# Optimization experiments

Hardware: AMD Instinct MI355X
Metric: run time of the kernel (lower is better)

## Reference

```python
import jax, jax.numpy as jnp
import numpy as np

B, N, IN, OUT, H = 8, 256, 256, 256, 4
HD = OUT // H  # 64
ALPHA = 0.2    # LeakyReLU negative slope
EPS = 1e-5


def layernorm(x, g, b):
    m = x.mean(-1, keepdims=True)
    v = jnp.mean(jnp.square(x - m), axis=-1, keepdims=True)
    return (x - m) / jnp.sqrt(v + EPS) * g + b


def setup_inputs() -> dict:
    key = jax.random.key(0)
    ks = jax.random.split(key, 16)
    s = 0.05
    return {
        'h':    jax.random.normal(ks[0], (B, N, IN), jnp.float32),
        'adj':  jax.random.randint(ks[1], (B, N, N), 0, 2, jnp.int32),
        # per-head params (leading dim H)
        'W':    jax.random.normal(ks[2], (H, IN, HD), jnp.float32) * s,      # node proj (no bias)
        'We1':  jax.random.normal(ks[3], (H, 2 * IN, HD), jnp.float32) * s,  # edge_encoder lin
        'be1':  jnp.zeros((H, HD), jnp.float32),
        'Wa1':  jax.random.normal(ks[4], (H, 3 * HD, HD), jnp.float32) * s,  # attn mlp lin1
        'ba1':  jnp.zeros((H, HD), jnp.float32),
        'wa2':  jax.random.normal(ks[5], (H, HD), jnp.float32) * s,          # attn mlp lin2 -> scalar
        'ba2':  jnp.zeros((H,), jnp.float32),
        'ln_g': jnp.ones((H, HD), jnp.float32),   # per-head LayerNorm
        'ln_b': jnp.zeros((H, HD), jnp.float32),
        'Wo':   jax.random.normal(ks[6], (OUT, OUT), jnp.float32) * s,       # output projection
        'bo':   jnp.zeros((OUT,), jnp.float32),
        'ln2_g': jnp.ones((OUT,), jnp.float32),   # final LayerNorm
        'ln2_b': jnp.zeros((OUT,), jnp.float32),
    }


def _head(h, adj_mask, W, We1, be1, Wa1, ba1, wa2, ba2, g, b):
    # h: [B,N,IN]; adj_mask: [B,N,N] bool (True where adj==0)
    Wh = jnp.einsum('bnf,fd->bnd', h, W)                      # [B,N,HD]
    # attention MLP lin1 applied to concat([Wh_i, Wh_j, edge]):
    # split weight so the per-node parts are computed once, broadcast over pairs
    Wa, Wb, We = Wa1[:HD], Wa1[HD:2 * HD], Wa1[2 * HD:]
    si = jnp.einsum('bnd,de->bne', Wh, Wa) + ba1              # [B,N,HD]
    sj = jnp.einsum('bnd,de->bne', Wh, Wb)                    # [B,N,HD]
    # edge encoder: Linear(cat[h_i,h_j]) -> leaky_relu, split likewise
    ei = jnp.einsum('bnf,fd->bnd', h, We1[:IN]) + be1         # [B,N,HD]
    ej = jnp.einsum('bnf,fd->bnd', h, We1[IN:])               # [B,N,HD]
    edge = jax.nn.leaky_relu(ei[:, :, None, :] + ej[:, None, :, :], ALPHA)  # [B,N,N,HD]
    hidden = jax.nn.leaky_relu(
        si[:, :, None, :] + sj[:, None, :, :] + jnp.einsum('bijd,de->bije', edge, We),
        ALPHA)                                                # [B,N,N,HD]
    e = jnp.einsum('bijd,d->bij', hidden, wa2) + ba2          # [B,N,N]
    e = jnp.where(adj_mask, -1e9, e)
    attn = jax.nn.softmax(e, axis=-1)                         # [B,N,N]
    hp = jnp.einsum('bij,bjd->bid', attn, Wh)                 # [B,N,HD]
    return layernorm(hp, g, b)


def reference(h, adj, W, We1, be1, Wa1, ba1, wa2, ba2, ln_g, ln_b, Wo, bo, ln2_g, ln2_b):
    adj_mask = (adj == 0)
    heads = [
        _head(h, adj_mask, W[i], We1[i], be1[i], Wa1[i], ba1[i],
              wa2[i], ba2[i], ln_g[i], ln_b[i])
        for i in range(H)
    ]
    concat = jnp.concatenate(heads, axis=-1)                  # [B,N,OUT]
    out = jnp.einsum('bnf,fo->bno', concat, Wo) + bo
    out = out + h                                             # residual (IN == OUT)
    return layernorm(out, ln2_g, ln2_b)
```

## Files before the change

### kernel.cpp

```cpp
#include <hip/hip_runtime.h>
#include <hip/hip_bf16.h>

#define B_ 8
#define N_ 256
#define IN_ 256
#define OUT_ 256
#define H_ 4
#define HD_ 64
#define ALPHA_ 0.2f
#define EPS_ 1e-5f

#define S_ (B_*H_*N_*HD_)


typedef unsigned short ushort_t;
typedef __attribute__((ext_vector_type(8))) short short8;
typedef __attribute__((ext_vector_type(4))) float floatx4;

__device__ __forceinline__ float lrelu(float x) { return fmaxf(x, ALPHA_ * x); }
__device__ __forceinline__ ushort_t f2b(float x) {
    unsigned u = __float_as_uint(x);
    unsigned r = ((u >> 16) & 1u) + 0x7fffu;
    return (ushort_t)((u + r) >> 16);
}
__device__ __forceinline__ unsigned pk2(float x0, float x1) {
    __hip_bfloat162 p = __float22bfloat162_rn(make_float2(x0, x1));
    return *(unsigned*)&p;
}

__global__ __launch_bounds__(256) void build_kernel(
    const float* __restrict__ W, const float* __restrict__ We1,
    const float* __restrict__ Wa1, const float* __restrict__ Wo,
    ushort_t* __restrict__ wfull, ushort_t* __restrict__ wo_t,
    ushort_t* __restrict__ bw_b)
{
    const int blk = blockIdx.x;
    const int tid = threadIdx.x;
    const int r4 = tid >> 6, cl = tid & 63;

    if (blk < 48) {
        const int hh = blk / 12, rem = blk % 12;
        const int cq = rem >> 2, ft = rem & 3;
        const int f0 = ft * 64;
        __shared__ float tl[64][65];
        for (int r = r4; r < 64; r += 4) {
            float v;
            if (cq == 0)      v = W  [((size_t)hh * 256 + f0 + r) * 64 + cl];
            else if (cq == 1) v = We1[((size_t)hh * 512 + f0 + r) * 64 + cl];
            else              v = We1[((size_t)hh * 512 + 256 + f0 + r) * 64 + cl];
            tl[r][cl] = v;
        }
        __syncthreads();
        for (int cr = r4; cr < 64; cr += 4)
            wfull[((size_t)hh * 256 + cq * 64 + cr) * 256 + f0 + cl] = f2b(tl[cl][cr]);
    } else if (blk < 64) {
        const int mm = blk - 48;
        const int hh = mm >> 2, ft = mm & 3;
        const int f0 = ft * 64;
        __shared__ float wlds[64][65];
        __shared__ float wa_l[64][65];
        __shared__ float tl[64][65];
        for (int r = r4; r < 64; r += 4) {
            wlds[r][cl] = W[((size_t)hh * 256 + f0 + r) * 64 + cl];
            wa_l[r][cl] = Wa1[((size_t)hh * 192 + r) * 64 + cl];
        }
        __syncthreads();
        for (int f = r4; f < 64; f += 4) {
            float acc = 0.f;
            #pragma unroll 8
            for (int g = 0; g < 64; ++g) acc += wlds[f][g] * wa_l[g][cl];
            tl[f][cl] = acc;
        }
        __syncthreads();
        for (int cr = r4; cr < 64; cr += 4)
            wfull[((size_t)hh * 256 + 192 + cr) * 256 + f0 + cl] = f2b(tl[cl][cr]);
    } else if (blk < 80) {
        const int bb = blk - 64;
        const int to = bb & 3, tf = bb >> 2;
        __shared__ float t[64][65];
        for (int rr = r4; rr < 64; rr += 4)
            t[rr][cl] = Wo[(size_t)(tf * 64 + rr) * 256 + to * 64 + cl];
        __syncthreads();
        for (int rr = r4; rr < 64; rr += 4)
            wo_t[(size_t)(to * 64 + rr) * 256 + tf * 64 + cl] = f2b(t[cl][rr]);
    } else {
        const int hh = blk - 80;
        for (int idx = tid; idx < 64 * 128; idx += 256) {
            const int e = idx >> 7, k = idx & 127;
            const int row = (k < 64) ? (128 + k) : k;
            bw_b[hh * 8192 + idx] = f2b(Wa1[(size_t)hh * 192 * 64 + row * 64 + e]);
        }
    }
}

__global__ __launch_bounds__(256) void prep2_kernel(
    const float* __restrict__ h, const ushort_t* __restrict__ wfull,
    const float* __restrict__ be1, const float* __restrict__ ba1,
    float* __restrict__ ws)
{
    const int gm = blockIdx.x & 127, gn = blockIdx.x >> 7;
    const int tid = threadIdx.x, lane = tid & 63, wid = tid >> 6;
    const int quad = lane >> 4, l15 = lane & 15;

    float*    ei_f = ws;
    float*    si_f = ws + S_;
    ushort_t* ej_b = (ushort_t*)(ws + 2 * (size_t)S_);
    ushort_t* Wh_b = ej_b + S_;

    floatx4 acc[2];
    #pragma unroll
    for (int nt = 0; nt < 2; ++nt) acc[nt] = (floatx4){0.f,0.f,0.f,0.f};

    #pragma unroll 2
    for (int ks = 0; ks < 8; ++ks) {
        const float* hp0 = &h[(size_t)(gm * 16 + l15) * 256 + ks * 32 + quad * 8];
        float4 a0 = *(const float4*)hp0;
        float4 a1 = *(const float4*)(hp0 + 4);
        union { unsigned u[4]; short8 s; } aw;
        aw.u[0] = pk2(a0.x, a0.y); aw.u[1] = pk2(a0.z, a0.w);
        aw.u[2] = pk2(a1.x, a1.y); aw.u[3] = pk2(a1.z, a1.w);
        #pragma unroll
        for (int nt = 0; nt < 2; ++nt) {
            short8 bfr = *(const short8*)&wfull[(size_t)(gn * 128 + wid * 32 + nt * 16 + l15) * 256 + ks * 32 + quad * 8];
            acc[nt] = __builtin_amdgcn_mfma_f32_16x16x32_bf16(aw.s, bfr, acc[nt], 0, 0, 0);
        }
    }

    #pragma unroll
    for (int nt = 0; nt < 2; ++nt) {
        const int colg = gn * 128 + wid * 32 + nt * 16 + l15;
        const int head = colg >> 8, c = colg & 255, type = c >> 6, d = c & 63;
        #pragma unroll
        for (int reg = 0; reg < 4; ++reg) {
            const int row = gm * 16 + quad * 4 + reg;
            const int b = row >> 8, n = row & 255;
            const size_t idx = ((size_t)(b * H_ + head) * 256 + n) * 64 + d;
            const float v = acc[nt][reg];
            if      (type == 0) Wh_b[idx] = f2b(v);
            else if (type == 1) ei_f[idx] = v + be1[head * 64 + d];
            else if (type == 2) ej_b[idx] = f2b(v);
            else                si_f[idx] = v + ba1[head * 64 + d];
        }
    }
}

__global__ __launch_bounds__(256, 2) void attn_kernel(
    const int* __restrict__ adj, const float* __restrict__ wa2,
    const float* __restrict__ ba2, const float* __restrict__ ln_g,
    const float* __restrict__ ln_b, float* __restrict__ ws)
{
    const int blk  = blockIdx.x;
    const int ig   = blk & 15;
    const int head = (blk >> 4) & 3;
    const int b    = blk >> 6;
    const int i0   = ig * 16;
    const int tid  = threadIdx.x;
    const int lane = tid & 63;
    const int wid  = tid >> 6;
    const int quad = lane >> 4;
    const int l15  = lane & 15;
    const int bh   = b * H_ + head;

    __shared__ float    P_s[16 * 256];
    __shared__ ushort_t Pb_s[16 * 264];
    __shared__ float    ei_s[16 * 64];
    __shared__ float    si_s[16 * 64];
    __shared__ unsigned long long adjm_s[16 * 4];
    __shared__ float    hp_s[16 * 68];

    const float*    ei_f = ws;
    const float*    si_f = ws + S_;
    const ushort_t* ej_b = (const ushort_t*)(ws + 2 * (size_t)S_);
    const ushort_t* Wh_b = ej_b + S_;
    ushort_t*       conc = (ushort_t*)(ws + 3 * (size_t)S_) + 524288;
    const ushort_t* bw_b = (const ushort_t*)(ws + 4 * (size_t)S_) + 262144 + 65536;

    {
        const int ii = tid >> 4, c = tid & 15;
        *(float4*)&ei_s[ii * 64 + c * 4] =
            *(const float4*)&ei_f[((size_t)(bh * 256 + i0 + ii)) * 64 + c * 4];
        *(float4*)&si_s[ii * 64 + c * 4] =
            *(const float4*)&si_f[((size_t)(bh * 256 + i0 + ii)) * 64 + c * 4];
    }
    {
        int av[16];
        #pragma unroll
        for (int r = 0; r < 16; ++r)
            av[r] = adj[((size_t)(b * 256 + i0 + r)) * 256 + tid];
        #pragma unroll
        for (int r = 0; r < 16; ++r) {
            unsigned long long mk = __ballot(av[r] != 0);
            if (lane == 0) adjm_s[r * 4 + wid] = mk;
        }
    }

    uint4   ejr[4][2];
    short8  afrWe[4][2];
    floatx4 sjaccT[4][4];
    float   w6[4][4], w4[4][4];
    #pragma unroll
    for (int nt = 0; nt < 4; ++nt) {
        const size_t jrow = (size_t)(bh * 256 + wid * 64 + nt * 16 + l15) * 64;
        #pragma unroll
        for (int kk = 0; kk < 2; ++kk)
            ejr[nt][kk] = *(const uint4*)&ej_b[jrow + kk * 32 + quad * 8];
    }
    #pragma unroll
    for (int mt = 0; mt < 4; ++mt) {
        #pragma unroll
        for (int ks = 0; ks < 2; ++ks)
            afrWe[mt][ks] = *(const short8*)&bw_b[head * 8192 + (mt * 16 + l15) * 128 + ks * 32 + quad * 8];
        float4 wvv = *(const float4*)&wa2[head * 64 + mt * 16 + quad * 4];
        w6[mt][0] = 0.6f * wvv.x; w4[mt][0] = 0.4f * wvv.x;
        w6[mt][1] = 0.6f * wvv.y; w4[mt][1] = 0.4f * wvv.y;
        w6[mt][2] = 0.6f * wvv.z; w4[mt][2] = 0.4f * wvv.z;
        w6[mt][3] = 0.6f * wvv.w; w4[mt][3] = 0.4f * wvv.w;
    }
    {
        #pragma unroll
        for (int mt = 0; mt < 4; ++mt)
            #pragma unroll
            for (int nt = 0; nt < 4; ++nt) sjaccT[mt][nt] = (floatx4){0.f,0.f,0.f,0.f};
        #pragma unroll
        for (int ks = 2; ks < 4; ++ks) {
            short8 aWb[4], bWh[4];
            #pragma unroll
            for (int mt = 0; mt < 4; ++mt)
                aWb[mt] = *(const short8*)&bw_b[head * 8192 + (mt * 16 + l15) * 128 + ks * 32 + quad * 8];
            #pragma unroll
            for (int nt = 0; nt < 4; ++nt)
                bWh[nt] = *(const short8*)&Wh_b[((size_t)(bh * 256 + wid * 64 + nt * 16 + l15)) * 64
                                                + (ks - 2) * 32 + quad * 8];
            #pragma unroll
            for (int mt = 0; mt < 4; ++mt)
                #pragma unroll
                for (int nt = 0; nt < 4; ++nt)
                    sjaccT[mt][nt] = __builtin_amdgcn_mfma_f32_16x16x32_bf16(
                        aWb[mt], bWh[nt], sjaccT[mt][nt], 0, 0, 0);
        }
    }
    const float ba2h = ba2[head];

    __syncthreads();

    for (int i = 0; i < 16; ++i) {
        floatx4 acc[4][4];
        #pragma unroll
        for (int ks = 0; ks < 2; ++ks) {
            short8 tfr[4];
            float ev[8];
            *(float4*)&ev[0] = *(const float4*)&ei_s[i * 64 + ks * 32 + quad * 8];
            *(float4*)&ev[4] = *(const float4*)&ei_s[i * 64 + ks * 32 + quad * 8 + 4];
            #pragma unroll
            for (int nt = 0; nt < 4; ++nt) {
                const unsigned* rw = (const unsigned*)&ejr[nt][ks];
                union { unsigned u[4]; short8 s; } ow;
                #pragma unroll
                for (int p = 0; p < 4; ++p) {
                    float x0 = __uint_as_float(rw[p] << 16)         + ev[2 * p];
                    float x1 = __uint_as_float(rw[p] & 0xffff0000u) + ev[2 * p + 1];
                    ow.u[p] = pk2(lrelu(x0), lrelu(x1));
                }
                tfr[nt] = ow.s;
            }
            if (ks == 0) {
                #pragma unroll
                for (int mt = 0; mt < 4; ++mt)
                    #pragma unroll
                    for (int nt = 0; nt < 4; ++nt)
                        acc[mt][nt] = __builtin_amdgcn_mfma_f32_16x16x32_bf16(
                            afrWe[mt][0], tfr[nt], sjaccT[mt][nt], 0, 0, 0);
            } else {
                #pragma unroll
                for (int mt = 0; mt < 4; ++mt)
                    #pragma unroll
                    for (int nt = 0; nt < 4; ++nt)
                        acc[mt][nt] = __builtin_amdgcn_mfma_f32_16x16x32_bf16(
                            afrWe[mt][1], tfr[nt], acc[mt][nt], 0, 0, 0);
            }
        }

        float sv[4][4];
        #pragma unroll
        for (int mt = 0; mt < 4; ++mt)
            *(float4*)&sv[mt][0] = *(const float4*)&si_s[i * 64 + mt * 16 + quad * 4];
        #pragma unroll
        for (int nt = 0; nt < 4; ++nt) {
            float val = 0.f;
            #pragma unroll
            for (int mt = 0; mt < 4; ++mt)
                #pragma unroll
                for (int reg = 0; reg < 4; ++reg) {
                    const float t = acc[mt][nt][reg] + sv[mt][reg];
                    val = fmaf(t, w6[mt][reg], val);
                    val = fmaf(fabsf(t), w4[mt][reg], val);
                }
            val += __shfl_xor(val, 16, 64);
            val += __shfl_xor(val, 32, 64);
            if (quad == 0)
                P_s[i * 256 + wid * 64 + nt * 16 + l15] = val + ba2h;
        }
    }
    __syncthreads();

    #pragma unroll
    for (int rr = 0; rr < 4; ++rr) {
        const int r = rr * 4 + wid;
        float4 v = *(const float4*)&P_s[r * 256 + lane * 4];
        const unsigned mk = (unsigned)(adjm_s[r * 4 + quad] >> (l15 * 4)) & 0xFu;
        float v0 = (mk & 1u) ? v.x : -1e9f;
        float v1 = (mk & 2u) ? v.y : -1e9f;
        float v2 = (mk & 4u) ? v.z : -1e9f;
        float v3 = (mk & 8u) ? v.w : -1e9f;
        float m = fmaxf(fmaxf(v0, v1), fmaxf(v2, v3));
        #pragma unroll
        for (int off = 32; off >= 1; off >>= 1) m = fmaxf(m, __shfl_xor(m, off, 64));
        float p0 = __expf(v0 - m), p1 = __expf(v1 - m);
        float p2 = __expf(v2 - m), p3 = __expf(v3 - m);
        float s = (p0 + p1) + (p2 + p3);
        #pragma unroll
        for (int off = 32; off >= 1; off >>= 1) s += __shfl_xor(s, off, 64);
        const float inv = 1.f / s;
        uint2 o; o.x = pk2(p0 * inv, p1 * inv); o.y = pk2(p2 * inv, p3 * inv);
        *(uint2*)&Pb_s[r * 264 + lane * 4] = o;
    }
    __syncthreads();

    floatx4 hacc = (floatx4){0.f,0.f,0.f,0.f};
    #pragma unroll
    for (int s = 0; s < 8; ++s) {
        short8 af = *(const short8*)&Pb_s[l15 * 264 + s * 32 + quad * 8];
        short8 bf;
        #pragma unroll
        for (int jj = 0; jj < 8; ++jj)
            bf[jj] = (short)Wh_b[((size_t)(bh * 256) + s * 32 + quad * 8 + jj) * 64 + wid * 16 + l15];
        hacc = __builtin_amdgcn_mfma_f32_16x16x32_bf16(af, bf, hacc, 0, 0, 0);
    }
    #pragma unroll
    for (int reg = 0; reg < 4; ++reg)
        hp_s[(quad * 4 + reg) * 68 + wid * 16 + l15] = hacc[reg];
    __syncthreads();

    const float gg = ln_g[head * 64 + lane];
    const float bb = ln_b[head * 64 + lane];
    #pragma unroll
    for (int pss = 0; pss < 4; ++pss) {
        const int r = pss * 4 + wid;
        const float v = hp_s[r * 68 + lane];
        float s1 = v, s2 = v * v;
        #pragma unroll
        for (int off = 32; off >= 1; off >>= 1) {
            s1 += __shfl_xor(s1, off, 64);
            s2 += __shfl_xor(s2, off, 64);
        }
        const float mean = s1 * (1.f / 64.f);
        const float var = s2 * (1.f / 64.f) - mean * mean;
        const float o = (v - mean) * __frsqrt_rn(var + EPS_) * gg + bb;
        conc[((size_t)(b * 256 + i0 + r)) * 256 + head * 64 + lane] = f2b(o);
    }
}

__global__ __launch_bounds__(256) void out2_kernel(
    const float* __restrict__ h, const float* __restrict__ bo,
    const float* __restrict__ ln2_g, const float* __restrict__ ln2_b,
    const ushort_t* __restrict__ conc, const ushort_t* __restrict__ wo_t,
    float* __restrict__ out)
{
    const int rowbase = blockIdx.x * 8;
    const int tid = threadIdx.x, lane = tid & 63, wid = tid >> 6;
    const int quad = lane >> 4, l15 = lane & 15;

    __shared__ float s1a[8][4], s2a[8][4];

    floatx4 acc[4];
    #pragma unroll
    for (int nt = 0; nt < 4; ++nt) acc[nt] = (floatx4){0.f,0.f,0.f,0.f};

    #pragma unroll 2
    for (int ks = 0; ks < 8; ++ks) {
        short8 afr = *(const short8*)&conc[(size_t)(rowbase + (l15 & 7)) * 256 + ks * 32 + quad * 8];
        #pragma unroll
        for (int nt = 0; nt < 4; ++nt) {
            short8 bfr = *(const short8*)&wo_t[(size_t)(wid * 64 + nt * 16 + l15) * 256 + ks * 32 + quad * 8];
            acc[nt] = __builtin_amdgcn_mfma_f32_16x16x32_bf16(afr, bfr, acc[nt], 0, 0, 0);
        }
    }

    float x[4][4];
    if (quad < 2) {
        float s1[4], s2[4];
        #pragma unroll
        for (int reg = 0; reg < 4; ++reg) { s1[reg] = 0.f; s2[reg] = 0.f; }
        #pragma unroll
        for (int nt = 0; nt < 4; ++nt) {
            const int col = wid * 64 + nt * 16 + l15;
            const float bv = bo[col];
            #pragma unroll
            for (int reg = 0; reg < 4; ++reg) {
                const int row = rowbase + quad * 4 + reg;
                float v = acc[nt][reg] + bv + h[(size_t)row * 256 + col];
                x[nt][reg] = v;
                s1[reg] += v;
                s2[reg] += v * v;
            }
        }
        #pragma unroll
        for (int reg = 0; reg < 4; ++reg) {
            #pragma unroll
            for (int off = 1; off <= 8; off <<= 1) {
                s1[reg] += __shfl_xor(s1[reg], off, 64);
                s2[reg] += __shfl_xor(s2[reg], off, 64);
            }
            if (l15 == 0) {
                s1a[quad * 4 + reg][wid] = s1[reg];
                s2a[quad * 4 + reg][wid] = s2[reg];
            }
        }
    }
    __syncthreads();

    if (quad < 2) {
        #pragma unroll
        for (int reg = 0; reg < 4; ++reg) {
            const int r = quad * 4 + reg;
            const float S1 = s1a[r][0] + s1a[r][1] + s1a[r][2] + s1a[r][3];
            const float S2 = s2a[r][0] + s2a[r][1] + s2a[r][2] + s2a[r][3];
            const float mean = S1 * (1.f / 256.f);
            const float var = S2 * (1.f / 256.f) - mean * mean;
            const float rs = __frsqrt_rn(var + EPS_);
            const int row = rowbase + r;
            #pragma unroll
            for (int nt = 0; nt < 4; ++nt) {
                const int col = wid * 64 + nt * 16 + l15;
                out[(size_t)row * 256 + col] =
                    (x[nt][reg] - mean) * rs * ln2_g[col] + ln2_b[col];
            }
        }
    }
}

extern "C" void kernel_launch(void* const* d_in, const int* in_sizes, int n_in,
                              void* d_out, int out_size, void* d_ws, size_t ws_size,
                              hipStream_t stream)
{
    const float* h    = (const float*)d_in[0];
    const int*   adj  = (const int*)  d_in[1];
    const float* W    = (const float*)d_in[2];
    const float* We1  = (const float*)d_in[3];
    const float* be1  = (const float*)d_in[4];
    const float* Wa1  = (const float*)d_in[5];
    const float* ba1  = (const float*)d_in[6];
    const float* wa2  = (const float*)d_in[7];
    const float* ba2  = (const float*)d_in[8];
    const float* ln_g = (const float*)d_in[9];
    const float* ln_b = (const float*)d_in[10];
    const float* Wo   = (const float*)d_in[11];
    const float* bo   = (const float*)d_in[12];
    const float* ln2g = (const float*)d_in[13];
    const float* ln2b = (const float*)d_in[14];

    float* ws = (float*)d_ws;
    ushort_t* conc  = (ushort_t*)(ws + 3 * (size_t)S_) + 524288;
    ushort_t* wfull = (ushort_t*)(ws + 4 * (size_t)S_);
    ushort_t* wo_t  = wfull + 262144;
    ushort_t* bw_b  = wo_t + 65536;
    float* out = (float*)d_out;

    build_kernel<<<84,   256, 0, stream>>>(W, We1, Wa1, Wo, wfull, wo_t, bw_b);
    prep2_kernel<<<1024, 256, 0, stream>>>(h, wfull, be1, ba1, ws);
    attn_kernel <<<512,  256, 0, stream>>>(adj, wa2, ba2, ln_g, ln_b, ws);
    out2_kernel <<<256,  256, 0, stream>>>(h, bo, ln2g, ln2b, conc, wo_t, out);
}
```

Baseline: 176.6 us.

## Drop weight-prep kernel; read fp32 weights directly and compute si inside attention

Removes the build_kernel launch that pre-transposed and converted weights to bf16. Consumers now gather fp32 weight columns with strided loads and pack them to bf16 on the fly. The si = Wh·Wa projection, previously folded into the prep GEMM through a precomputed W·Wa product, is now computed per tile with MFMA inside attn_kernel. This shrinks the prep GEMM from 1024 to 768 blocks and saves one launch plus the si workspace traffic. In exchange it adds uncoalesced strided fp32 weight loads in every block and changes rounding, since si now goes through bf16 Wh rather than a fused fp32 weight product.

```diff
diff --git a/kernel.cpp b/kernel.cpp
--- a/kernel.cpp
+++ b/kernel.cpp
@@ -27,75 +27,18 @@
     __hip_bfloat162 p = __float22bfloat162_rn(make_float2(x0, x1));
     return *(unsigned*)&p;
 }
-
-__global__ __launch_bounds__(256) void build_kernel(
-    const float* __restrict__ W, const float* __restrict__ We1,
-    const float* __restrict__ Wa1, const float* __restrict__ Wo,
-    ushort_t* __restrict__ wfull, ushort_t* __restrict__ wo_t,
-    ushort_t* __restrict__ bw_b)
-{
-    const int blk = blockIdx.x;
-    const int tid = threadIdx.x;
-    const int r4 = tid >> 6, cl = tid & 63;
-
-    if (blk < 48) {
-        const int hh = blk / 12, rem = blk % 12;
-        const int cq = rem >> 2, ft = rem & 3;
-        const int f0 = ft * 64;
-        __shared__ float tl[64][65];
-        for (int r = r4; r < 64; r += 4) {
-            float v;
-            if (cq == 0)      v = W  [((size_t)hh * 256 + f0 + r) * 64 + cl];
-            else if (cq == 1) v = We1[((size_t)hh * 512 + f0 + r) * 64 + cl];
-            else              v = We1[((size_t)hh * 512 + 256 + f0 + r) * 64 + cl];
-            tl[r][cl] = v;
-        }
-        __syncthreads();
-        for (int cr = r4; cr < 64; cr += 4)
-            wfull[((size_t)hh * 256 + cq * 64 + cr) * 256 + f0 + cl] = f2b(tl[cl][cr]);
-    } else if (blk < 64) {
-        const int mm = blk - 48;
-        const int hh = mm >> 2, ft = mm & 3;
-        const int f0 = ft * 64;
-        __shared__ float wlds[64][65];
-        __shared__ float wa_l[64][65];
-        __shared__ float tl[64][65];
-        for (int r = r4; r < 64; r += 4) {
-            wlds[r][cl] = W[((size_t)hh * 256 + f0 + r) * 64 + cl];
-            wa_l[r][cl] = Wa1[((size_t)hh * 192 + r) * 64 + cl];
-        }
-        __syncthreads();
-        for (int f = r4; f < 64; f += 4) {
-            float acc = 0.f;
-            #pragma unroll 8
-            for (int g = 0; g < 64; ++g) acc += wlds[f][g] * wa_l[g][cl];
-            tl[f][cl] = acc;
-        }
-        __syncthreads();
-        for (int cr = r4; cr < 64; cr += 4)
-            wfull[((size_t)hh * 256 + 192 + cr) * 256 + f0 + cl] = f2b(tl[cl][cr]);
-    } else if (blk < 80) {
-        const int bb = blk - 64;
-        const int to = bb & 3, tf = bb >> 2;
-        __shared__ float t[64][65];
-        for (int rr = r4; rr < 64; rr += 4)
-            t[rr][cl] = Wo[(size_t)(tf * 64 + rr) * 256 + to * 64 + cl];
-        __syncthreads();
-        for (int rr = r4; rr < 64; rr += 4)
-            wo_t[(size_t)(to * 64 + rr) * 256 + tf * 64 + cl] = f2b(t[cl][rr]);
-    } else {
-        const int hh = blk - 80;
-        for (int idx = tid; idx < 64 * 128; idx += 256) {
-            const int e = idx >> 7, k = idx & 127;
-            const int row = (k < 64) ? (128 + k) : k;
-            bw_b[hh * 8192 + idx] = f2b(Wa1[(size_t)hh * 192 * 64 + row * 64 + e]);
-        }
-    }
+template<int STRIDE>
+__device__ __forceinline__ short8 gcol(const float* __restrict__ base) {
+    union { unsigned u[4]; short8 s; } w;
+    #pragma unroll
+    for (int p = 0; p < 4; ++p)
+        w.u[p] = pk2(base[(2 * p) * STRIDE], base[(2 * p + 1) * STRIDE]);
+    return w.s;
 }
 
 __global__ __launch_bounds__(256) void prep2_kernel(
-    const float* __restrict__ h, const ushort_t* __restrict__ wfull,
-    const float* __restrict__ be1, const float* __restrict__ ba1,
+    const float* __restrict__ h, const float* __restrict__ W,
+    const float* __restrict__ We1, const float* __restrict__ be1,
     float* __restrict__ ws)
 {
     const int gm = blockIdx.x & 127, gn = blockIdx.x >> 7;
@@ -103,9 +46,22 @@
     const int quad = lane >> 4, l15 = lane & 15;
 
     float*    ei_f = ws;
-    float*    si_f = ws + S_;
-    ushort_t* ej_b = (ushort_t*)(ws + 2 * (size_t)S_);
+    ushort_t* ej_b = (ushort_t*)(ws + S_);
     ushort_t* Wh_b = ej_b + S_;
+
+    int headA[2], typeA[2], dA[2];
+    const float* wbase[2];
+    #pragma unroll
+    for (int nt = 0; nt < 2; ++nt) {
+        const int colg = gn * 128 + wid * 32 + nt * 16 + l15;
+        const int head = colg / 192;
+        const int c    = colg - head * 192;
+        const int type = c >> 6, d = c & 63;
+        headA[nt] = head; typeA[nt] = type; dA[nt] = d;
+        if (type == 0)      wbase[nt] = W   + (size_t)head * 16384 + d;
+        else if (type == 1) wbase[nt] = We1 + (size_t)head * 32768 + d;
+        else                wbase[nt] = We1 + (size_t)head * 32768 + 16384 + d;
+    }
 
     floatx4 acc[2];
     #pragma unroll
@@ -121,15 +77,14 @@
         aw.u[2] = pk2(a1.x, a1.y); aw.u[3] = pk2(a1.z, a1.w);
         #pragma unroll
         for (int nt = 0; nt < 2; ++nt) {
-            short8 bfr = *(const short8*)&wfull[(size_t)(gn * 128 + wid * 32 + nt * 16 + l15) * 256 + ks * 32 + quad * 8];
+            short8 bfr = gcol<64>(wbase[nt] + (size_t)(ks * 32 + quad * 8) * 64);
             acc[nt] = __builtin_amdgcn_mfma_f32_16x16x32_bf16(aw.s, bfr, acc[nt], 0, 0, 0);
         }
     }
 
     #pragma unroll
     for (int nt = 0; nt < 2; ++nt) {
-        const int colg = gn * 128 + wid * 32 + nt * 16 + l15;
-        const int head = colg >> 8, c = colg & 255, type = c >> 6, d = c & 63;
+        const int head = headA[nt], type = typeA[nt], d = dA[nt];
         #pragma unroll
         for (int reg = 0; reg < 4; ++reg) {
             const int row = gm * 16 + quad * 4 + reg;
@@ -138,14 +93,14 @@
             const float v = acc[nt][reg];
             if      (type == 0) Wh_b[idx] = f2b(v);
             else if (type == 1) ei_f[idx] = v + be1[head * 64 + d];
-            else if (type == 2) ej_b[idx] = f2b(v);
-            else                si_f[idx] = v + ba1[head * 64 + d];
+            else                ej_b[idx] = f2b(v);
         }
     }
 }
 
 __global__ __launch_bounds__(256, 2) void attn_kernel(
-    const int* __restrict__ adj, const float* __restrict__ wa2,
+    const int* __restrict__ adj, const float* __restrict__ Wa1,
+    const float* __restrict__ ba1, const float* __restrict__ wa2,
     const float* __restrict__ ba2, const float* __restrict__ ln_g,
     const float* __restrict__ ln_b, float* __restrict__ ws)
 {
@@ -169,18 +124,15 @@
     __shared__ float    hp_s[16 * 68];
 
     const float*    ei_f = ws;
-    const float*    si_f = ws + S_;
-    const ushort_t* ej_b = (const ushort_t*)(ws + 2 * (size_t)S_);
+    const ushort_t* ej_b = (const ushort_t*)(ws + S_);
     const ushort_t* Wh_b = ej_b + S_;
-    ushort_t*       conc = (ushort_t*)(ws + 3 * (size_t)S_) + 524288;
-    const ushort_t* bw_b = (const ushort_t*)(ws + 4 * (size_t)S_) + 262144 + 65536;
+    ushort_t*       conc = (ushort_t*)(ws + 2 * (size_t)S_);
+    const float*    wa_base = Wa1 + (size_t)head * 12288;
 
     {
         const int ii = tid >> 4, c = tid & 15;
         *(float4*)&ei_s[ii * 64 + c * 4] =
             *(const float4*)&ei_f[((size_t)(bh * 256 + i0 + ii)) * 64 + c * 4];
-        *(float4*)&si_s[ii * 64 + c * 4] =
-            *(const float4*)&si_f[((size_t)(bh * 256 + i0 + ii)) * 64 + c * 4];
     }
     {
         int av[16];
@@ -209,7 +161,8 @@
     for (int mt = 0; mt < 4; ++mt) {
         #pragma unroll
         for (int ks = 0; ks < 2; ++ks)
-            afrWe[mt][ks] = *(const short8*)&bw_b[head * 8192 + (mt * 16 + l15) * 128 + ks * 32 + quad * 8];
+            afrWe[mt][ks] = gcol<64>(wa_base + (size_t)(128 + ks * 32 + quad * 8) * 64
+                                     + mt * 16 + l15);
         float4 wvv = *(const float4*)&wa2[head * 64 + mt * 16 + quad * 4];
         w6[mt][0] = 0.6f * wvv.x; w4[mt][0] = 0.4f * wvv.x;
         w6[mt][1] = 0.6f * wvv.y; w4[mt][1] = 0.4f * wvv.y;
@@ -226,7 +179,8 @@
             short8 aWb[4], bWh[4];
             #pragma unroll
             for (int mt = 0; mt < 4; ++mt)
-                aWb[mt] = *(const short8*)&bw_b[head * 8192 + (mt * 16 + l15) * 128 + ks * 32 + quad * 8];
+                aWb[mt] = gcol<64>(wa_base + (size_t)(64 + (ks - 2) * 32 + quad * 8) * 64
+                                   + mt * 16 + l15);
             #pragma unroll
             for (int nt = 0; nt < 4; ++nt)
                 bWh[nt] = *(const short8*)&Wh_b[((size_t)(bh * 256 + wid * 64 + nt * 16 + l15)) * 64
@@ -238,6 +192,21 @@
                     sjaccT[mt][nt] = __builtin_amdgcn_mfma_f32_16x16x32_bf16(
                         aWb[mt], bWh[nt], sjaccT[mt][nt], 0, 0, 0);
         }
+    }
+    {
+        floatx4 siacc = (floatx4){0.f,0.f,0.f,0.f};
+        #pragma unroll
+        for (int ks = 0; ks < 2; ++ks) {
+            short8 aWh = *(const short8*)&Wh_b[((size_t)(bh * 256 + i0 + l15)) * 64
+                                               + ks * 32 + quad * 8];
+            short8 bWa = gcol<64>(wa_base + (size_t)(ks * 32 + quad * 8) * 64
+                                  + wid * 16 + l15);
+            siacc = __builtin_amdgcn_mfma_f32_16x16x32_bf16(aWh, bWa, siacc, 0, 0, 0);
+        }
+        const float ba1v = ba1[head * 64 + wid * 16 + l15];
+        #pragma unroll
+        for (int reg = 0; reg < 4; ++reg)
+            si_s[(quad * 4 + reg) * 64 + wid * 16 + l15] = siacc[reg] + ba1v;
     }
     const float ba2h = ba2[head];
 
@@ -361,9 +330,9 @@
 }
 
 __global__ __launch_bounds__(256) void out2_kernel(
-    const float* __restrict__ h, const float* __restrict__ bo,
-    const float* __restrict__ ln2_g, const float* __restrict__ ln2_b,
-    const ushort_t* __restrict__ conc, const ushort_t* __restrict__ wo_t,
+    const float* __restrict__ h, const float* __restrict__ Wo,
+    const float* __restrict__ bo, const float* __restrict__ ln2_g,
+    const float* __restrict__ ln2_b, const ushort_t* __restrict__ conc,
     float* __restrict__ out)
 {
     const int rowbase = blockIdx.x * 8;
@@ -381,7 +350,8 @@
         short8 afr = *(const short8*)&conc[(size_t)(rowbase + (l15 & 7)) * 256 + ks * 32 + quad * 8];
         #pragma unroll
         for (int nt = 0; nt < 4; ++nt) {
-            short8 bfr = *(const short8*)&wo_t[(size_t)(wid * 64 + nt * 16 + l15) * 256 + ks * 32 + quad * 8];
+            short8 bfr = gcol<256>(Wo + (size_t)(ks * 32 + quad * 8) * 256
+                                   + wid * 64 + nt * 16 + l15);
             acc[nt] = __builtin_amdgcn_mfma_f32_16x16x32_bf16(afr, bfr, acc[nt], 0, 0, 0);
         }
     }
@@ -460,14 +430,10 @@
     const float* ln2b = (const float*)d_in[14];
 
     float* ws = (float*)d_ws;
-    ushort_t* conc  = (ushort_t*)(ws + 3 * (size_t)S_) + 524288;
-    ushort_t* wfull = (ushort_t*)(ws + 4 * (size_t)S_);
-    ushort_t* wo_t  = wfull + 262144;
-    ushort_t* bw_b  = wo_t + 65536;
+    ushort_t* conc = (ushort_t*)(ws + 2 * (size_t)S_);
     float* out = (float*)d_out;
 
-    build_kernel<<<84,   256, 0, stream>>>(W, We1, Wa1, Wo, wfull, wo_t, bw_b);
-    prep2_kernel<<<1024, 256, 0, stream>>>(h, wfull, be1, ba1, ws);
-    attn_kernel <<<512,  256, 0, stream>>>(adj, wa2, ba2, ln_g, ln_b, ws);
-    out2_kernel <<<256,  256, 0, stream>>>(h, bo, ln2g, ln2b, conc, wo_t, out);
-}
+    prep2_kernel<<<768, 256, 0, stream>>>(h, W, We1, be1, ws);
+    attn_kernel <<<512, 256, 0, stream>>>(adj, Wa1, ba1, wa2, ba2, ln_g, ln_b, ws);
+    out2_kernel <<<256, 256, 0, stream>>>(h, Wo, bo, ln2g, ln2b, conc, out);
+}
```

After: 155.3 us, median of 2. 1.14x faster.
